# Kernel tuning notes

Measured on AMD Instinct MI355X. Metric: run time of the kernel, lower is better.

Reference implementation:

```python
import jax, jax.numpy as jnp
import numpy as np

N_NEIGHBORS = 15
N_BATCHES = 3
TEMPERATURE = 1.0
DISTANCE_MASK_SENTINEL = 1e10  # pushes self-distance out of the neighborhood
EPS = 1e-8


def setup_inputs() -> dict:
    key = jax.random.key(0)
    k1, k2 = jax.random.split(key)
    embeddings = jax.random.normal(k1, (8192, 512), dtype=jnp.float32)
    batch_labels = jax.random.randint(k2, (8192,), 0, N_BATCHES, dtype=jnp.int32)
    return {"embeddings": embeddings, "batch_labels": batch_labels}


def reference(embeddings, batch_labels):
    n_cells = embeddings.shape[0]
    # pairwise squared euclidean distances: [n, n]
    sq_norms = jnp.sum(embeddings ** 2, axis=-1)
    distances = sq_norms[:, None] + sq_norms[None, :] - 2.0 * (embeddings @ embeddings.T)
    distances = distances + jnp.eye(n_cells, dtype=distances.dtype) * DISTANCE_MASK_SENTINEL

    # soft neighbor weights
    neighbor_weights = jax.nn.softmax(-distances / TEMPERATURE, axis=-1)

    # differentiable sort along rows (jnp.sort is piecewise-linear, differentiable)
    sorted_dists = jnp.sort(distances, axis=-1)
    kth_dist = sorted_dists[:, N_NEIGHBORS - 1:N_NEIGHBORS]  # [n, 1]

    # soft less(distances, kth_dist): sigmoid((kth - d) / softness)
    k_mask = jax.nn.sigmoid((kth_dist - distances) / TEMPERATURE)

    neighbor_weights = neighbor_weights * k_mask
    neighbor_weights = neighbor_weights / (neighbor_weights.sum(axis=-1, keepdims=True) + EPS)

    # batch distribution in each soft neighborhood: [n, n_batches]
    batch_onehot = jax.nn.one_hot(batch_labels, N_BATCHES, dtype=neighbor_weights.dtype)
    batch_dist = neighbor_weights @ batch_onehot

    per_cell_entropy = -jnp.sum(batch_dist * jnp.log(batch_dist + EPS), axis=-1)
    max_entropy = jnp.log(jnp.asarray(N_BATCHES, dtype=jnp.float32))
    normalized_entropy = per_cell_entropy / (max_entropy + EPS)
    return -jnp.mean(normalized_entropy)
```

## Files before the change

kernel.cpp:

```cpp
#include <hip/hip_runtime.h>
#include <math.h>

#define N_CELLS 8192
#define DIM 512
#define TILE 128
#define BK 64
#define KITERS (DIM / BK)
#define NSTRIPE (N_CELLS / TILE)
#define NTRI (NSTRIPE * (NSTRIPE + 1) / 2)
#define SAMPLE 1024
#define CAP 384
#define WQCAP 1024

typedef float f32x4 __attribute__((ext_vector_type(4)));
typedef _Float16 f16x8 __attribute__((ext_vector_type(8)));

#define AS1U(p) ((const __attribute__((address_space(1))) unsigned int*)(p))
#define AS3U(p) ((__attribute__((address_space(3))) unsigned int*)(p))

__device__ __forceinline__ unsigned fkey(float f) {
    unsigned u = __float_as_uint(f);
    return (u & 0x80000000u) ? ~u : (u | 0x80000000u);
}
__device__ __forceinline__ float finv(unsigned k) {
    unsigned u = (k & 0x80000000u) ? (k ^ 0x80000000u) : ~k;
    return __uint_as_float(u);
}

__global__ __launch_bounds__(256) void prep_kernel(const float* __restrict__ E,
                                                   unsigned short* __restrict__ Efp,
                                                   float* __restrict__ norms,
                                                   float* __restrict__ out) {
    if (blockIdx.x == 0 && threadIdx.x == 0) out[0] = 0.0f;
    const int wave = threadIdx.x >> 6, lane = threadIdx.x & 63;
    const int row = blockIdx.x * 4 + wave;
    const float4* e4 = (const float4*)(E + (size_t)row * DIM);
    float4 a = e4[lane * 2], b = e4[lane * 2 + 1];
    f16x8 h;
    h[0] = (_Float16)a.x; h[1] = (_Float16)a.y; h[2] = (_Float16)a.z; h[3] = (_Float16)a.w;
    h[4] = (_Float16)b.x; h[5] = (_Float16)b.y; h[6] = (_Float16)b.z; h[7] = (_Float16)b.w;
    const int kc = lane >> 3;
    const int u  = lane & 7;
    *(f16x8*)(Efp + ((size_t)kc * N_CELLS + row) * 64 + (size_t)(u ^ (row & 7)) * 8) = h;
    float s = a.x*a.x + a.y*a.y + a.z*a.z + a.w*a.w
            + b.x*b.x + b.y*b.y + b.z*b.z + b.w*b.w;
    #pragma unroll
    for (int off = 32; off > 0; off >>= 1) s += __shfl_down(s, off, 64);
    if (lane == 0) norms[row] = s;
}

__global__ __launch_bounds__(256) void norms_kernel(const float* __restrict__ E,
                                                    float* __restrict__ norms,
                                                    float* __restrict__ out) {
    if (blockIdx.x == 0 && threadIdx.x == 0) out[0] = 0.0f;
    const int wave = threadIdx.x >> 6, lane = threadIdx.x & 63;
    const int row = blockIdx.x * 4 + wave;
    const float4* e4 = (const float4*)(E + (size_t)row * DIM);
    float4 a = e4[lane], b = e4[lane + 64];
    float s = a.x*a.x + a.y*a.y + a.z*a.z + a.w*a.w
            + b.x*b.x + b.y*b.y + b.z*b.z + b.w*b.w;
    #pragma unroll
    for (int off = 32; off > 0; off >>= 1) s += __shfl_down(s, off, 64);
    if (lane == 0) norms[row] = s;
}


#define STAGE_PACKED(it)                                                                          \
    do {                                                                                          \
        const unsigned short* pa_ = Efp + ((size_t)(it) * N_CELLS + arow) * 64;                   \
        const unsigned short* pb_ = Efp + ((size_t)(it) * N_CELLS + brow) * 64;                   \
        _Pragma("unroll")                                                                         \
        for (int q_ = 0; q_ < 4; q_++) {                                                          \
            __builtin_amdgcn_global_load_lds(AS1U(pa_ + q_*2048 + t*8),                           \
                                             AS3U(smem + q_*4096 + t*16), 16, 0, 0);              \
            __builtin_amdgcn_global_load_lds(AS1U(pb_ + q_*2048 + t*8),                           \
                                             AS3U(smem + 16384 + q_*4096 + t*16), 16, 0, 0);      \
        }                                                                                         \
    } while (0)

#define GEMM_COMPUTE()                                                                            \
    do {                                                                                          \
        _Pragma("unroll")                                                                         \
        for (int ks = 0; ks < 2; ks++) {                                                          \
            f16x8 af[4], bf[4];                                                                   \
            _Pragma("unroll")                                                                     \
            for (int tm = 0; tm < 4; tm++)                                                        \
                af[tm] = *(const f16x8*)(smem + (size_t)(wr*64 + tm*16 + fr) * 128                \
                                              + (((ks*4 + kg) * 16) ^ fx));                       \
            _Pragma("unroll")                                                                     \
            for (int tn = 0; tn < 4; tn++)                                                        \
                bf[tn] = *(const f16x8*)(smem + 16384 + (size_t)(wc*64 + tn*16 + fr) * 128        \
                                              + (((ks*4 + kg) * 16) ^ fx));                       \
            _Pragma("unroll")                                                                     \
            for (int tm = 0; tm < 4; tm++)                                                        \
                _Pragma("unroll")                                                                 \
                for (int tn = 0; tn < 4; tn++)                                                    \
                    acc[tm][tn] = __builtin_amdgcn_mfma_f32_16x16x32_f16(af[tm], bf[tn],          \
                                                                         acc[tm][tn], 0, 0, 0);  \
        }                                                                                         \
    } while (0)

#define GEMM_LOOP()                                                                               \
    do {                                                                                          \
        _Pragma("unroll")                                                                         \
        for (int it = 0; it < KITERS; ++it) {                                                     \
            __syncthreads();                                                                      \
            STAGE_PACKED(it);                                                                     \
            __syncthreads();                                                                      \
            GEMM_COMPUTE();                                                                       \
        }                                                                                         \
        __syncthreads();                                                                          \
    } while (0)

__global__ __launch_bounds__(256) void samp_dist_kernel(const unsigned short* __restrict__ Efp,
                                                        const float* __restrict__ norms,
                                                        float* __restrict__ Dsamp) {
    __shared__ __align__(16) char smem[32768];

    const int t = threadIdx.x;
    const int lane = t & 63;
    const int w = t >> 6;
    const int wr = w >> 1, wc = w & 1;

    const int arow = blockIdx.y * TILE;
    const int brow = blockIdx.x * TILE;

    const int kg = lane >> 4;
    const int fr = lane & 15;
    const int fx = (fr & 7) << 4;

    f32x4 acc[4][4];
    #pragma unroll
    for (int a = 0; a < 4; a++)
        #pragma unroll
        for (int b = 0; b < 4; b++)
            acc[a][b] = (f32x4){0.f, 0.f, 0.f, 0.f};

    GEMM_LOOP();

    const int colb = brow + wc * 64 + fr;
    const int rowb = arow + wr * 64 + (lane >> 4) * 4;
    #pragma unroll
    for (int tn = 0; tn < 4; tn++) {
        const int col = colb + tn * 16;
        const float nj = norms[col];
        #pragma unroll
        for (int tm = 0; tm < 4; tm++) {
            #pragma unroll
            for (int r = 0; r < 4; r++) {
                const int row = rowb + tm * 16 + r;
                float d = norms[row] + nj - 2.0f * acc[tm][tn][r];
                if (row == col) d += 1e10f;
                Dsamp[(size_t)row * SAMPLE + col] = d;
            }
        }
    }
}

__global__ __launch_bounds__(256) void tsel_kernel(const float* __restrict__ Dsamp,
                                                   float* __restrict__ T,
                                                   int* __restrict__ cnt) {
    const int row = blockIdx.x * 4 + (threadIdx.x >> 6);
    const int lane = threadIdx.x & 63;
    const float4* r4 = (const float4*)(Dsamp + (size_t)row * SAMPLE);

    float v[16];
    #pragma unroll
    for (int s = 0; s < 4; s++) {
        float4 d4 = r4[s * 64 + lane];
        v[s*4+0] = d4.x; v[s*4+1] = d4.y; v[s*4+2] = d4.z; v[s*4+3] = d4.w;
    }
    #pragma unroll
    for (int k = 2; k <= 16; k <<= 1) {
        #pragma unroll
        for (int j = k >> 1; j > 0; j >>= 1) {
            #pragma unroll
            for (int i = 0; i < 16; i++) {
                const int l = i ^ j;
                if (l > i) {
                    const bool up = ((i & k) == 0);
                    const float a = v[i], b = v[l];
                    v[i] = up ? fminf(a, b) : fmaxf(a, b);
                    v[l] = up ? fmaxf(a, b) : fminf(a, b);
                }
            }
        }
    }
    float m0 = v[0], m14 = v[14];
    #pragma unroll
    for (int off = 32; off > 0; off >>= 1) {
        m0  = fminf(m0,  __shfl_down(m0,  off, 64));
        m14 = fminf(m14, __shfl_down(m14, off, 64));
    }
    m0  = __shfl(m0,  0, 64);
    m14 = __shfl(m14, 0, 64);

    unsigned lo = fkey(m0), hi = fkey(m14);
    int it = 0;
    while (lo < hi && it < 34) {
        it++;
        const unsigned mid = lo + ((hi - lo) >> 1);
        const float fm = finv(mid);
        int c = 0;
        #pragma unroll
        for (int k = 0; k < 16; k++) c += (v[k] <= fm) ? 1 : 0;
        #pragma unroll
        for (int off = 32; off > 0; off >>= 1) c += __shfl_down(c, off, 64);
        c = __shfl(c, 0, 64);
        if (c >= 15) hi = mid; else lo = mid + 1;
    }
    if (lane == 0) { T[row] = finv(lo); cnt[row] = 0; }
}

__global__ __launch_bounds__(256) void main_cand_kernel(const unsigned short* __restrict__ Efp,
                                                        const float* __restrict__ norms,
                                                        const int* __restrict__ labels,
                                                        const float* __restrict__ T,
                                                        int* __restrict__ cnt,
                                                        int2* __restrict__ cand) {
    __shared__ __align__(16) char smem[32768];

    const int t = threadIdx.x;
    const int lane = t & 63;
    const int w = t >> 6;
    const int wr = w >> 1, wc = w & 1;

    const int fid = blockIdx.x;
    const int y = fid / 65;
    const int x = fid - y * 65;
    const int a = (x <= y) ? y : (NSTRIPE - 1 - y);
    const int b = (x <= y) ? x : (x - y - 1);

    const int arow = a * TILE;
    const int brow = b * TILE;
    const bool diag = (a == b);

    const int kg = lane >> 4;
    const int fr = lane & 15;
    const int fx = (fr & 7) << 4;

    f32x4 acc[4][4];
    #pragma unroll
    for (int aa = 0; aa < 4; aa++)
        #pragma unroll
        for (int bb = 0; bb < 4; bb++)
            acc[aa][bb] = (f32x4){0.f, 0.f, 0.f, 0.f};

    GEMM_LOOP();

    int2* wq = (int2*)(smem + (size_t)w * 8192);

    const int colb = brow + wc * 64 + fr;
    const int rowb = arow + wr * 64 + (lane >> 4) * 4;

    float Trow[4][4], Nrow[4][4];
    int Lrow[4][4];
    #pragma unroll
    for (int tm = 0; tm < 4; tm++)
        #pragma unroll
        for (int r = 0; r < 4; r++) {
            const int row = rowb + tm * 16 + r;
            Trow[tm][r] = T[row];
            Nrow[tm][r] = norms[row];
            Lrow[tm][r] = labels[row];
        }
    float Tcol[4];
    #pragma unroll
    for (int tn = 0; tn < 4; tn++) Tcol[tn] = T[colb + tn * 16];

    int wn = 0;
    #pragma unroll
    for (int tn = 0; tn < 4; tn++) {
        const int col = colb + tn * 16;
        const float nj = norms[col];
        const int labc = labels[col];
        #pragma unroll
        for (int tm = 0; tm < 4; tm++) {
            #pragma unroll
            for (int r = 0; r < 4; r++) {
                const int row = rowb + tm * 16 + r;
                const float d = Nrow[tm][r] + nj - 2.0f * acc[tm][tn][r];
                const bool live = !diag || (row > col);
                {
                    const bool hit = live && (d <= Trow[tm][r]);
                    const unsigned long long bal = __ballot(hit);
                    if (hit) {
                        const int pos = __popcll(bal & ((1ull << lane) - 1ull));
                        if (wn + pos < WQCAP)
                            wq[wn + pos] = make_int2(__float_as_int(d), row | (labc << 13));
                    }
                    wn += (int)__popcll(bal);
                }
                {
                    const bool hit = live && (d <= Tcol[tn]);
                    const unsigned long long bal = __ballot(hit);
                    if (hit) {
                        const int pos = __popcll(bal & ((1ull << lane) - 1ull));
                        if (wn + pos < WQCAP)
                            wq[wn + pos] = make_int2(__float_as_int(d), col | (Lrow[tm][r] << 13));
                    }
                    wn += (int)__popcll(bal);
                }
            }
        }
    }

    const int qn = (wn < WQCAP) ? wn : WQCAP;
    for (int i = lane; i < qn; i += 64) {
        const int2 e = wq[i];
        const int row = e.y & 8191;
        const int lab = e.y >> 13;
        const int idx = atomicAdd(&cnt[row], 1);
        if (idx < CAP) cand[(size_t)row * CAP + idx] = make_int2(e.x, lab);
    }
    if (wn > WQCAP)
        for (int r2 = lane; r2 < TILE; r2 += 64) {
            atomicAdd(&cnt[arow + r2], 1000000);
            atomicAdd(&cnt[brow + r2], 1000000);
        }
}

__global__ __launch_bounds__(256) void final_kernel(const int2* __restrict__ cand,
                                                    const int* __restrict__ cnt,
                                                    const float* __restrict__ T,
                                                    float* __restrict__ rowloss) {
    const int row = blockIdx.x * 4 + (threadIdx.x >> 6);
    const int lane = threadIdx.x & 63;
    const int n = cnt[row];
    if (n < 15 || n > CAP) return;

    float d[CAP / 64];
    int lb[CAP / 64];
    #pragma unroll
    for (int s = 0; s < CAP / 64; s++) {
        const int idx = s * 64 + lane;
        if (idx < n) {
            const int2 c = cand[(size_t)row * CAP + idx];
            d[s] = __int_as_float(c.x);
            lb[s] = c.y;
        } else { d[s] = 3.0e38f; lb[s] = 3; }
    }

    float dmin = d[0];
    #pragma unroll
    for (int s = 1; s < CAP / 64; s++) dmin = fminf(dmin, d[s]);
    #pragma unroll
    for (int off = 32; off > 0; off >>= 1) dmin = fminf(dmin, __shfl_down(dmin, off, 64));
    dmin = __shfl(dmin, 0, 64);

    unsigned lo = fkey(dmin), hi = fkey(T[row]);
    int it = 0;
    while (lo < hi && it < 34) {
        it++;
        const unsigned mid = lo + ((hi - lo) >> 1);
        const float fm = finv(mid);
        int c = 0;
        #pragma unroll
        for (int s = 0; s < CAP / 64; s++) c += (d[s] <= fm) ? 1 : 0;
        #pragma unroll
        for (int off = 32; off > 0; off >>= 1) c += __shfl_down(c, off, 64);
        c = __shfl(c, 0, 64);
        if (c >= 15) hi = mid; else lo = mid + 1;
    }
    const float kth = finv(lo);

    float z = 0.f, s0 = 0.f, s1 = 0.f, s2 = 0.f;
    #pragma unroll
    for (int s = 0; s < CAP / 64; s++) {
        const float w = __expf(dmin - d[s]);
        const float msk = 1.0f / (1.0f + __expf(d[s] - kth));
        const float p = w * msk;
        z  += w;
        s0 += (lb[s] == 0) ? p : 0.f;
        s1 += (lb[s] == 1) ? p : 0.f;
        s2 += (lb[s] == 2) ? p : 0.f;
    }
    #pragma unroll
    for (int off = 32; off > 0; off >>= 1) {
        z  += __shfl_down(z,  off, 64);
        s0 += __shfl_down(s0, off, 64);
        s1 += __shfl_down(s1, off, 64);
        s2 += __shfl_down(s2, off, 64);
    }
    if (lane == 0) {
        const float ssum = s0 + s1 + s2;
        const float denom = ssum + 1e-8f * z;
        const float q0 = s0/denom, q1 = s1/denom, q2 = s2/denom;
        const float H = -(q0*logf(q0+1e-8f) + q1*logf(q1+1e-8f) + q2*logf(q2+1e-8f));
        rowloss[row] = -(H / (logf(3.0f) + 1e-8f)) * (1.0f / N_CELLS);
    }
}

__global__ __launch_bounds__(512) void reduce_kernel(const float* __restrict__ rowloss,
                                                     float* __restrict__ out) {
    __shared__ float wsum[8];
    const int t = threadIdx.x, lane = t & 63, wv = t >> 6;
    const float4* r4 = (const float4*)rowloss;
    float s = 0.f;
    for (int i = t; i < N_CELLS / 4; i += 512) {
        const float4 v = r4[i];
        s += v.x + v.y + v.z + v.w;
    }
    #pragma unroll
    for (int off = 32; off > 0; off >>= 1) s += __shfl_down(s, off, 64);
    if (lane == 0) wsum[wv] = s;
    __syncthreads();
    if (t == 0) {
        float tot = 0.f;
        #pragma unroll
        for (int i = 0; i < 8; i++) tot += wsum[i];
        out[0] = tot;
    }
}

template<int NT>
__device__ __forceinline__ void finish_row(const float* rowb,
                                           float lst[15],
                                           const int* __restrict__ labels,
                                           float* __restrict__ out,
                                           float* __restrict__ rowloss,
                                           int rowidx) {
    constexpr int WAVES = NT / 64;
    __shared__ float w0s[WAVES], w14s[WAVES];
    __shared__ int cnt;
    __shared__ float zz[WAVES], r0s[WAVES], r1s[WAVES], r2s[WAVES];

    const int t = threadIdx.x;
    const int lane = t & 63, wave = t >> 6;

    float m0 = lst[0], m14 = lst[14];
    #pragma unroll
    for (int off = 32; off > 0; off >>= 1) {
        m0  = fminf(m0,  __shfl_down(m0,  off, 64));
        m14 = fminf(m14, __shfl_down(m14, off, 64));
    }
    if (lane == 0) { w0s[wave] = m0; w14s[wave] = m14; }
    __syncthreads();
    float dmin = w0s[0], ub = w14s[0];
    #pragma unroll
    for (int i = 1; i < WAVES; i++) { dmin = fminf(dmin, w0s[i]); ub = fminf(ub, w14s[i]); }

    unsigned lo = fkey(dmin), hi = fkey(ub);
    int iter = 0;
    while (lo < hi && iter < 34) {
        iter++;
        const unsigned mid = lo + ((hi - lo) >> 1);
        const float fmid = finv(mid);
        int c = 0;
        #pragma unroll
        for (int k = 0; k < 15; k++) c += (lst[k] <= fmid) ? 1 : 0;
        #pragma unroll
        for (int off = 32; off > 0; off >>= 1) c += __shfl_down(c, off, 64);
        __syncthreads();
        if (t == 0) cnt = 0;
        __syncthreads();
        if (lane == 0) atomicAdd(&cnt, c);
        __syncthreads();
        const int total = cnt;
        if (total >= 15) hi = mid; else lo = mid + 1;
    }
    const float kth = finv(hi);

    const float4* rb4 = (const float4*)rowb;
    const int4* lb4 = (const int4*)labels;
    float z = 0.f, s0 = 0.f, s1 = 0.f, s2 = 0.f;
    #pragma unroll
    for (int s = 0; s < N_CELLS / (4 * NT); s++) {
        const int idx = s * NT + t;
        const float4 d4 = rb4[idx];
        const int4 l4 = lb4[idx];
        #pragma unroll
        for (int c2 = 0; c2 < 4; c2++) {
            const float d = (c2 == 0) ? d4.x : (c2 == 1) ? d4.y : (c2 == 2) ? d4.z : d4.w;
            const int lab = (c2 == 0) ? l4.x : (c2 == 1) ? l4.y : (c2 == 2) ? l4.z : l4.w;
            const float w = __expf(dmin - d);
            const float msk = 1.0f / (1.0f + __expf(d - kth));
            const float p = w * msk;
            z  += w;
            s0 += (lab == 0) ? p : 0.f;
            s1 += (lab == 1) ? p : 0.f;
            s2 += (lab == 2) ? p : 0.f;
        }
    }
    #pragma unroll
    for (int off = 32; off > 0; off >>= 1) {
        z  += __shfl_down(z,  off, 64);
        s0 += __shfl_down(s0, off, 64);
        s1 += __shfl_down(s1, off, 64);
        s2 += __shfl_down(s2, off, 64);
    }
    if (lane == 0) { zz[wave] = z; r0s[wave] = s0; r1s[wave] = s1; r2s[wave] = s2; }
    __syncthreads();
    if (t == 0) {
        float Z = 0.f, S0 = 0.f, S1 = 0.f, S2 = 0.f;
        #pragma unroll
        for (int i = 0; i < WAVES; i++) { Z += zz[i]; S0 += r0s[i]; S1 += r1s[i]; S2 += r2s[i]; }
        const float ssum = S0 + S1 + S2;
        const float denom = ssum + 1e-8f * Z;
        const float q0 = S0/denom, q1 = S1/denom, q2 = S2/denom;
        const float H = -(q0*logf(q0+1e-8f) + q1*logf(q1+1e-8f) + q2*logf(q2+1e-8f));
        const float contrib = -(H / (logf(3.0f) + 1e-8f)) * (1.0f / N_CELLS);
        if (rowloss) rowloss[rowidx] = contrib;
        else atomicAdd(out, contrib);
    }
}

__device__ void process_row(int i,
                            const float* __restrict__ E,
                            const float* __restrict__ norms,
                            const int* __restrict__ labels,
                            float* __restrict__ out,
                            float* __restrict__ rowloss,
                            float* rowb, float* ei) {
    const int t = threadIdx.x;
    __syncthreads();
    for (int k = t; k < DIM; k += 512) ei[k] = E[(size_t)i * DIM + k];
    __syncthreads();
    const float ni = norms[i];

    float lst[15];
    #pragma unroll
    for (int k = 0; k < 15; k++) lst[k] = 3.0e38f;

    for (int s = 0; s < N_CELLS / 512; s++) {
        const int j = s * 512 + t;
        const float* ej = E + (size_t)j * DIM;
        float dot = 0.f;
        #pragma unroll 4
        for (int k = 0; k < DIM; k += 4) {
            float4 e4 = *(const float4*)(ej + k);
            dot += ei[k]*e4.x + ei[k+1]*e4.y + ei[k+2]*e4.z + ei[k+3]*e4.w;
        }
        float d = ni + norms[j] - 2.0f * dot;
        if (j == i) d += 1e10f;
        rowb[j] = d;
        float v = d;
        #pragma unroll
        for (int k = 0; k < 15; k++) {
            float lo2 = fminf(lst[k], v);
            v = fmaxf(lst[k], v);
            lst[k] = lo2;
        }
    }
    finish_row<512>(rowb, lst, labels, out, rowloss, i);
}

__global__ __launch_bounds__(512) void fused_kernel(const float* __restrict__ E,
                                                    const float* __restrict__ norms,
                                                    const int* __restrict__ labels,
                                                    float* __restrict__ out,
                                                    float* __restrict__ rowloss,
                                                    const int* __restrict__ cnt_g) {
    __shared__ float rowb[N_CELLS];
    __shared__ float ei[DIM];
    __shared__ int bad[TILE];
    __shared__ int nbad;
    const int t = threadIdx.x;

    if (cnt_g == nullptr) {
        process_row(blockIdx.x, E, norms, labels, out, nullptr, rowb, ei);
        return;
    }
    if (t == 0) nbad = 0;
    __syncthreads();
    if (t < TILE) {
        const int row = blockIdx.x * TILE + t;
        const int n = cnt_g[row];
        if (n < 15 || n > CAP) bad[atomicAdd(&nbad, 1)] = row;
    }
    __syncthreads();
    const int nb = nbad;
    for (int b = 0; b < nb; b++)
        process_row(bad[b], E, norms, labels, out, rowloss, rowb, ei);
}

extern "C" void kernel_launch(void* const* d_in, const int* in_sizes, int n_in,
                              void* d_out, int out_size, void* d_ws, size_t ws_size,
                              hipStream_t stream) {
    const float* E = (const float*)d_in[0];
    const int* labels = (const int*)d_in[1];
    float* out = (float*)d_out;

    char* p = (char*)d_ws;
    float* norms = (float*)p;                 p += 32768;
    unsigned short* Efp = (unsigned short*)p; p += (size_t)N_CELLS * DIM * 2;
    float* T = (float*)p;                     p += 32768;
    int* cnt = (int*)p;                       p += 32768;
    float* rowloss = (float*)p;               p += 32768;
    float* Dsamp = (float*)p;                 p += (size_t)N_CELLS * SAMPLE * 4;
    int2* cand = (int2*)p;                    p += (size_t)N_CELLS * CAP * 8;
    const size_t need = (size_t)(p - (char*)d_ws);

    if (ws_size >= need) {
        prep_kernel<<<N_CELLS / 4, 256, 0, stream>>>(E, Efp, norms, out);
        samp_dist_kernel<<<dim3(SAMPLE / TILE, N_CELLS / TILE), 256, 0, stream>>>(Efp, norms, Dsamp);
        tsel_kernel<<<N_CELLS / 4, 256, 0, stream>>>(Dsamp, T, cnt);
        main_cand_kernel<<<NTRI, 256, 0, stream>>>(Efp, norms, labels, T, cnt, cand);
        final_kernel<<<N_CELLS / 4, 256, 0, stream>>>(cand, cnt, T, rowloss);
        fused_kernel<<<N_CELLS / TILE, 512, 0, stream>>>(E, norms, labels, out, rowloss, cnt);
        reduce_kernel<<<1, 512, 0, stream>>>(rowloss, out);
    } else {
        norms_kernel<<<N_CELLS / 4, 256, 0, stream>>>(E, norms, out);
        fused_kernel<<<N_CELLS, 512, 0, stream>>>(E, norms, labels, out, nullptr, nullptr);
    }
}
```

Baseline: 255.0 us.

## Enlarge GEMM tiles to 256x128 with 8 waves and remap triangular block indexing

Switches the sampled-distance and candidate GEMM kernels from 128x128 tiles with 4 waves to 256x128 tiles with 8 waves. The A tile is staged once per block and shared by more waves, which raises reuse and reduces global traffic per MFMA. The triangular block enumeration is redone for rectangular tiles using a sqrt-based index decode with a diagonal test. The per-wave candidate queue shrinks to fit the larger LDS footprint, which makes queue overflow and the fallback path more likely.

```diff
diff --git a/kernel.cpp b/kernel.cpp
--- a/kernel.cpp
+++ b/kernel.cpp
@@ -4,13 +4,15 @@
 #define N_CELLS 8192
 #define DIM 512
 #define TILE 128
+#define AM 256
+#define BN 128
 #define BK 64
 #define KITERS (DIM / BK)
-#define NSTRIPE (N_CELLS / TILE)
-#define NTRI (NSTRIPE * (NSTRIPE + 1) / 2)
+#define NSA (N_CELLS / AM)
+#define NTRI2 (NSA * NSA + NSA)
 #define SAMPLE 1024
 #define CAP 384
-#define WQCAP 1024
+#define WQCAP 768
 
 typedef float f32x4 __attribute__((ext_vector_type(4)));
 typedef _Float16 f16x8 __attribute__((ext_vector_type(8)));
@@ -70,12 +72,13 @@
         const unsigned short* pa_ = Efp + ((size_t)(it) * N_CELLS + arow) * 64;                   \
         const unsigned short* pb_ = Efp + ((size_t)(it) * N_CELLS + brow) * 64;                   \
         _Pragma("unroll")                                                                         \
-        for (int q_ = 0; q_ < 4; q_++) {                                                          \
-            __builtin_amdgcn_global_load_lds(AS1U(pa_ + q_*2048 + t*8),                           \
-                                             AS3U(smem + q_*4096 + t*16), 16, 0, 0);              \
-            __builtin_amdgcn_global_load_lds(AS1U(pb_ + q_*2048 + t*8),                           \
-                                             AS3U(smem + 16384 + q_*4096 + t*16), 16, 0, 0);      \
-        }                                                                                         \
+        for (int q_ = 0; q_ < 4; q_++)                                                            \
+            __builtin_amdgcn_global_load_lds(AS1U(pa_ + q_*4096 + t*8),                           \
+                                             AS3U(smem + q_*8192 + t*16), 16, 0, 0);              \
+        _Pragma("unroll")                                                                         \
+        for (int q_ = 0; q_ < 2; q_++)                                                            \
+            __builtin_amdgcn_global_load_lds(AS1U(pb_ + q_*4096 + t*8),                           \
+                                             AS3U(smem + 32768 + q_*8192 + t*16), 16, 0, 0);      \
     } while (0)
 
 #define GEMM_COMPUTE()                                                                            \
@@ -89,7 +92,7 @@
                                               + (((ks*4 + kg) * 16) ^ fx));                       \
             _Pragma("unroll")                                                                     \
             for (int tn = 0; tn < 4; tn++)                                                        \
-                bf[tn] = *(const f16x8*)(smem + 16384 + (size_t)(wc*64 + tn*16 + fr) * 128        \
+                bf[tn] = *(const f16x8*)(smem + 32768 + (size_t)(wc*64 + tn*16 + fr) * 128        \
                                               + (((ks*4 + kg) * 16) ^ fx));                       \
             _Pragma("unroll")                                                                     \
             for (int tm = 0; tm < 4; tm++)                                                        \
@@ -112,18 +115,18 @@
         __syncthreads();                                                                          \
     } while (0)
 
-__global__ __launch_bounds__(256) void samp_dist_kernel(const unsigned short* __restrict__ Efp,
+__global__ __launch_bounds__(512) void samp_dist_kernel(const unsigned short* __restrict__ Efp,
                                                         const float* __restrict__ norms,
                                                         float* __restrict__ Dsamp) {
-    __shared__ __align__(16) char smem[32768];
+    __shared__ __align__(16) char smem[49152];
 
     const int t = threadIdx.x;
     const int lane = t & 63;
     const int w = t >> 6;
     const int wr = w >> 1, wc = w & 1;
 
-    const int arow = blockIdx.y * TILE;
-    const int brow = blockIdx.x * TILE;
+    const int arow = blockIdx.y * AM;
+    const int brow = blockIdx.x * BN;
 
     const int kg = lane >> 4;
     const int fr = lane & 15;
@@ -212,13 +215,13 @@
     if (lane == 0) { T[row] = finv(lo); cnt[row] = 0; }
 }
 
-__global__ __launch_bounds__(256) void main_cand_kernel(const unsigned short* __restrict__ Efp,
+__global__ __launch_bounds__(512) void main_cand_kernel(const unsigned short* __restrict__ Efp,
                                                         const float* __restrict__ norms,
                                                         const int* __restrict__ labels,
                                                         const float* __restrict__ T,
                                                         int* __restrict__ cnt,
                                                         int2* __restrict__ cand) {
-    __shared__ __align__(16) char smem[32768];
+    __shared__ __align__(16) char smem[49152];
 
     const int t = threadIdx.x;
     const int lane = t & 63;
@@ -226,14 +229,14 @@
     const int wr = w >> 1, wc = w & 1;
 
     const int fid = blockIdx.x;
-    const int y = fid / 65;
-    const int x = fid - y * 65;
-    const int a = (x <= y) ? y : (NSTRIPE - 1 - y);
-    const int b = (x <= y) ? x : (x - y - 1);
-
-    const int arow = a * TILE;
-    const int brow = b * TILE;
-    const bool diag = (a == b);
+    int a = (int)((sqrtf(4.0f * (float)fid + 1.0f) - 1.0f) * 0.5f);
+    while ((a + 1) * (a + 2) <= fid) a++;
+    while (a * (a + 1) > fid) a--;
+    const int b = fid - a * (a + 1);
+
+    const int arow = a * AM;
+    const int brow = b * BN;
+    const bool diag = ((b >> 1) == a);
 
     const int kg = lane >> 4;
     const int fr = lane & 15;
@@ -248,7 +251,7 @@
 
     GEMM_LOOP();
 
-    int2* wq = (int2*)(smem + (size_t)w * 8192);
+    int2* wq = (int2*)(smem + (size_t)w * 6144);
 
     const int colb = brow + wc * 64 + fr;
     const int rowb = arow + wr * 64 + (lane >> 4) * 4;
@@ -313,11 +316,10 @@
         const int idx = atomicAdd(&cnt[row], 1);
         if (idx < CAP) cand[(size_t)row * CAP + idx] = make_int2(e.x, lab);
     }
-    if (wn > WQCAP)
-        for (int r2 = lane; r2 < TILE; r2 += 64) {
-            atomicAdd(&cnt[arow + r2], 1000000);
-            atomicAdd(&cnt[brow + r2], 1000000);
-        }
+    if (wn > WQCAP) {
+        for (int r2 = lane; r2 < AM; r2 += 64) atomicAdd(&cnt[arow + r2], 1000000);
+        for (int r2 = lane; r2 < BN; r2 += 64) atomicAdd(&cnt[brow + r2], 1000000);
+    }
 }
 
 __global__ __launch_bounds__(256) void final_kernel(const int2* __restrict__ cand,
@@ -593,9 +595,9 @@
 
     if (ws_size >= need) {
         prep_kernel<<<N_CELLS / 4, 256, 0, stream>>>(E, Efp, norms, out);
-        samp_dist_kernel<<<dim3(SAMPLE / TILE, N_CELLS / TILE), 256, 0, stream>>>(Efp, norms, Dsamp);
+        samp_dist_kernel<<<dim3(SAMPLE / BN, N_CELLS / AM), 512, 0, stream>>>(Efp, norms, Dsamp);
         tsel_kernel<<<N_CELLS / 4, 256, 0, stream>>>(Dsamp, T, cnt);
-        main_cand_kernel<<<NTRI, 256, 0, stream>>>(Efp, norms, labels, T, cnt, cand);
+        main_cand_kernel<<<NTRI2, 512, 0, stream>>>(Efp, norms, labels, T, cnt, cand);
         final_kernel<<<N_CELLS / 4, 256, 0, stream>>>(cand, cnt, T, rowloss);
         fused_kernel<<<N_CELLS / TILE, 512, 0, stream>>>(E, norms, labels, out, rowloss, cnt);
         reduce_kernel<<<1, 512, 0, stream>>>(rowloss, out);
```

Measured after the change: 261.9 us. 1.03x slower.
